# Performance work log

Measured on AMD Instinct MI355X. Metric: run time of the kernel, lower is better.

The kernel has to match this reference:

```python
import jax, jax.numpy as jnp
import numpy as np

NEG_INF = -1e15  # matches masked_fill value -1000000000000000.0
ALPHA = 0.2      # leakyReLU negative slope


def setup_inputs() -> dict:
    key = jax.random.key(0)
    k1, k2, k3, k4 = jax.random.split(key, 4)
    N, F_IN, F_OUT = 8192, 256, 64
    x = jax.random.normal(k1, (N, F_IN), dtype=jnp.float32)
    mask = jax.random.randint(k2, (N, N), 0, 2, dtype=jnp.int32)
    trans = jax.random.normal(k3, (F_IN, F_OUT), dtype=jnp.float32) * 0.1
    attn = jax.random.normal(k4, (2 * F_OUT, 1), dtype=jnp.float32) * 0.1
    return {"x": x, "mask": mask, "trans": trans, "attn": attn}


def reference(x, mask, trans, attn):
    d = trans.shape[1]
    h = x @ trans                                  # [N, d]
    e1 = h @ attn[:d, :]                           # [N, 1]
    e2 = h @ attn[d:, :]                           # [N, 1]
    scores = jax.nn.leaky_relu(e1 + e2.T, negative_slope=ALPHA)  # [N, N]
    masked = jnp.where(mask == 0, NEG_INF, scores)
    attention = jax.nn.softmax(masked, axis=1)
    return attention @ h                           # [N, d]
```

## Files before the change

### kernel.cpp

```cpp
#include <hip/hip_runtime.h>
#include <hip/hip_bf16.h>
#include <math.h>

#define N 8192
#define FIN 256
#define D 64
#define ALPHA 0.2f

typedef __attribute__((ext_vector_type(8))) short bf16x8;
typedef __attribute__((ext_vector_type(4))) float f32x4;

__global__ __launch_bounds__(256) void k_pack(
    const int* __restrict__ mask, unsigned char* __restrict__ mF)
{
    const int t = threadIdx.x;
    const int rt = blockIdx.x >> 1;
    const int half = blockIdx.x & 1;
    const int row = rt * 16 + (t >> 4);
    const int c = t & 15;
    const int m = t >> 4;
    for (int cc = half * (N / 2); cc < (half + 1) * (N / 2); cc += 128) {
        const int col = cc + c * 8;
        const int4 a = *(const int4*)(mask + (size_t)row * N + col);
        const int4 b = *(const int4*)(mask + (size_t)row * N + col + 4);
        unsigned v = (a.x != 0 ? 1u : 0u) | (a.y != 0 ? 2u : 0u)
                   | (a.z != 0 ? 4u : 0u) | (a.w != 0 ? 8u : 0u)
                   | (b.x != 0 ? 16u : 0u) | (b.y != 0 ? 32u : 0u)
                   | (b.z != 0 ? 64u : 0u) | (b.w != 0 ? 128u : 0u);
        const int cb = col >> 5;
        const int jgrp = c & 3;
        mF[((size_t)rt * 256 + cb) * 64 + jgrp * 16 + m] = (unsigned char)v;
    }
}

__global__ __launch_bounds__(256) void k_h_e(
    const float* __restrict__ x, const float* __restrict__ trans,
    const float* __restrict__ attn,
    __hip_bfloat16* __restrict__ hF, float* __restrict__ e1, float* __restrict__ e2)
{
    __shared__ float xs[8 * FIN];
    __shared__ __hip_bfloat16 hl[8 * D];
    const int t = threadIdx.x;
    const int r0 = blockIdx.x * 8;

    #pragma unroll
    for (int v = 0; v < 2; ++v) {
        int idx = t + 256 * v;
        ((float4*)xs)[idx] = ((const float4*)(x + (size_t)r0 * FIN))[idx];
    }
    __syncthreads();

    const int lane = t & 63, w = t >> 6;
    const float* xa = xs + (2 * w) * FIN;
    const float* xb = xs + (2 * w + 1) * FIN;
    float acca = 0.f, accb = 0.f;
    #pragma unroll 8
    for (int k = 0; k < FIN; ++k) {
        const float tv = trans[k * D + lane];
        acca = fmaf(xa[k], tv, acca);
        accb = fmaf(xb[k], tv, accb);
    }
    const int ra = r0 + 2 * w, rb = ra + 1;

    const float a1 = attn[lane], a2 = attn[D + lane];
    float p1a = acca * a1, p2a = acca * a2;
    float p1b = accb * a1, p2b = accb * a2;
    #pragma unroll
    for (int mm = 1; mm <= 32; mm <<= 1) {
        p1a += __shfl_xor(p1a, mm);
        p2a += __shfl_xor(p2a, mm);
        p1b += __shfl_xor(p1b, mm);
        p2b += __shfl_xor(p2b, mm);
    }
    if (lane == 0) { e1[ra] = p1a; e2[ra] = p2a; e1[rb] = p1b; e2[rb] = p2b; }

    hl[(2 * w) * D + lane]     = __float2bfloat16(acca);
    hl[(2 * w + 1) * D + lane] = __float2bfloat16(accb);
    __syncthreads();
    if (t < D) {
        const int q = t >> 4, m = t & 15;
        const int cb = r0 >> 5, jgrp = (r0 >> 3) & 3;
        union { bf16x8 v; __hip_bfloat16 h[8]; } o;
        #pragma unroll
        for (int r = 0; r < 8; ++r) o.h[r] = hl[r * D + q * 16 + m];
        *(bf16x8*)(hF + (((size_t)cb * 4 + q) * 64 + jgrp * 16 + m) * 8) = o.v;
    }
}

__global__ __launch_bounds__(256) void k_attn(
    const unsigned char* __restrict__ mF, const __hip_bfloat16* __restrict__ hF,
    const float* __restrict__ e1, const float* __restrict__ e2,
    float* __restrict__ acc_part, float* __restrict__ l_part, int cs)
{
    const int t = threadIdx.x;
    const int lane = t & 63, wave = t >> 6;
    const int i0 = (blockIdx.y * 4 + wave) * 16;
    const int rt = blockIdx.y * 4 + wave;
    const int sp = blockIdx.x;
    const int c0 = sp * cs;
    const int m = lane & 15, quad = lane >> 4;
    const int row = i0 + m;
    const float er = e1[row];

    const unsigned char* mbp = mF + ((size_t)rt * 256 + (c0 >> 5)) * 64 + lane;
    const __hip_bfloat16* hfp = hF + (((size_t)(c0 >> 5)) * 4 * 64 + lane) * 8;

    f32x4 acc0 = {0.f, 0.f, 0.f, 0.f};
    f32x4 acc1 = {0.f, 0.f, 0.f, 0.f};
    f32x4 acc2 = {0.f, 0.f, 0.f, 0.f};
    f32x4 acc3 = {0.f, 0.f, 0.f, 0.f};
    float lsum = 0.f;

    const int iters = cs >> 5;
    for (int it = 0; it < iters; ++it) {
        const int jb = c0 + it * 32 + quad * 8;
        const unsigned mc = mbp[it * 64];
        const float4 ea = *(const float4*)(e2 + jb);
        const float4 eb = *(const float4*)(e2 + jb + 4);
        const bf16x8* hq = (const bf16x8*)(hfp + (size_t)it * 2048);
        const bf16x8 b0 = hq[0];
        const bf16x8 b1 = hq[64];
        const bf16x8 b2 = hq[128];
        const bf16x8 b3 = hq[192];

        float s0 = er + ea.x; s0 = s0 > 0.f ? s0 : ALPHA * s0;
        float s1 = er + ea.y; s1 = s1 > 0.f ? s1 : ALPHA * s1;
        float s2 = er + ea.z; s2 = s2 > 0.f ? s2 : ALPHA * s2;
        float s3 = er + ea.w; s3 = s3 > 0.f ? s3 : ALPHA * s3;
        float s4 = er + eb.x; s4 = s4 > 0.f ? s4 : ALPHA * s4;
        float s5 = er + eb.y; s5 = s5 > 0.f ? s5 : ALPHA * s5;
        float s6 = er + eb.z; s6 = s6 > 0.f ? s6 : ALPHA * s6;
        float s7 = er + eb.w; s7 = s7 > 0.f ? s7 : ALPHA * s7;
        const float p0 = (mc & 1u)   ? __expf(s0) : 0.f;
        const float p1 = (mc & 2u)   ? __expf(s1) : 0.f;
        const float p2 = (mc & 4u)   ? __expf(s2) : 0.f;
        const float p3 = (mc & 8u)   ? __expf(s3) : 0.f;
        const float p4 = (mc & 16u)  ? __expf(s4) : 0.f;
        const float p5 = (mc & 32u)  ? __expf(s5) : 0.f;
        const float p6 = (mc & 64u)  ? __expf(s6) : 0.f;
        const float p7 = (mc & 128u) ? __expf(s7) : 0.f;

        union { bf16x8 v; __hip_bfloat162 h2[4]; } af;
        af.h2[0] = __float22bfloat162_rn(make_float2(p0, p1));
        af.h2[1] = __float22bfloat162_rn(make_float2(p2, p3));
        af.h2[2] = __float22bfloat162_rn(make_float2(p4, p5));
        af.h2[3] = __float22bfloat162_rn(make_float2(p6, p7));

        lsum += ((p0 + p1) + (p2 + p3)) + ((p4 + p5) + (p6 + p7));

        acc0 = __builtin_amdgcn_mfma_f32_16x16x32_bf16(af.v, b0, acc0, 0, 0, 0);
        acc1 = __builtin_amdgcn_mfma_f32_16x16x32_bf16(af.v, b1, acc1, 0, 0, 0);
        acc2 = __builtin_amdgcn_mfma_f32_16x16x32_bf16(af.v, b2, acc2, 0, 0, 0);
        acc3 = __builtin_amdgcn_mfma_f32_16x16x32_bf16(af.v, b3, acc3, 0, 0, 0);
    }

    lsum += __shfl_xor(lsum, 16);
    lsum += __shfl_xor(lsum, 32);
    if (quad == 0) l_part[(size_t)sp * N + row] = lsum;

    #pragma unroll
    for (int reg = 0; reg < 4; ++reg) {
        const size_t rbase = ((size_t)sp * N + i0 + quad * 4 + reg) * D;
        acc_part[rbase + m     ] = acc0[reg];
        acc_part[rbase + m + 16] = acc1[reg];
        acc_part[rbase + m + 32] = acc2[reg];
        acc_part[rbase + m + 48] = acc3[reg];
    }
}

__global__ __launch_bounds__(256) void k_reduce(
    const float* __restrict__ acc_part, const float* __restrict__ l_part,
    float* __restrict__ out, int nsplit)
{
    const int idx = blockIdx.x * 256 + threadIdx.x;
    const int row = idx >> 6;
    float sum = 0.f, l = 0.f;
    for (int s = 0; s < nsplit; ++s) {
        sum += acc_part[(size_t)s * N * D + idx];
        l   += l_part[(size_t)s * N + row];
    }
    out[idx] = sum / l;
}

extern "C" void kernel_launch(void* const* d_in, const int* in_sizes, int n_in,
                              void* d_out, int out_size, void* d_ws, size_t ws_size,
                              hipStream_t stream) {
    const float* x     = (const float*)d_in[0];
    const int*   mask  = (const int*)d_in[1];
    const float* trans = (const float*)d_in[2];
    const float* attn  = (const float*)d_in[3];
    float* out = (float*)d_out;

    char* ws = (char*)d_ws;
    __hip_bfloat16* hF = (__hip_bfloat16*)ws;
    char* p = ws + (size_t)D * N * sizeof(__hip_bfloat16);
    float* e1 = (float*)p;            p += (size_t)N * sizeof(float);
    float* e2 = (float*)p;            p += (size_t)N * sizeof(float);
    unsigned char* mF = (unsigned char*)p;  p += (size_t)N * (N / 8);

    const size_t used = (size_t)(p - ws);
    int nsplit = 8;
    while (nsplit > 1) {
        size_t need = used + (size_t)nsplit * N * sizeof(float)
                    + (size_t)nsplit * N * D * sizeof(float);
        if (need <= ws_size) break;
        nsplit >>= 1;
    }
    float* l_part = (float*)p;
    float* acc_part = l_part + (size_t)nsplit * N;

    k_pack<<<(N / 16) * 2, 256, 0, stream>>>(mask, mF);
    k_h_e<<<N / 8, 256, 0, stream>>>(x, trans, attn, hF, e1, e2);
    dim3 g2(nsplit, N / 64);
    k_attn<<<g2, 256, 0, stream>>>(mF, hF, e1, e2, acc_part, l_part, N / nsplit);
    k_reduce<<<(N * D) / 256, 256, 0, stream>>>(acc_part, l_part, out, nsplit);
}
```

Baseline: 427.7 us.

## Fuse mask reading into attention kernel and drop separate bit-pack pass

Removes the mask bit-packing kernel and has the attention kernel read the int32 mask directly with vector loads, so the 268MB mask goes through one pass instead of a read-then-write-then-read sequence. It also halves the column split count and unrolls the main loop by two. The attention loop now carries far more memory traffic per iteration and may become bandwidth-bound. Fewer splits reduce partial-sum traffic but also reduce grid parallelism.

```diff
diff --git a/kernel.cpp b/kernel.cpp
--- a/kernel.cpp
+++ b/kernel.cpp
@@ -9,29 +9,6 @@
 
 typedef __attribute__((ext_vector_type(8))) short bf16x8;
 typedef __attribute__((ext_vector_type(4))) float f32x4;
-
-__global__ __launch_bounds__(256) void k_pack(
-    const int* __restrict__ mask, unsigned char* __restrict__ mF)
-{
-    const int t = threadIdx.x;
-    const int rt = blockIdx.x >> 1;
-    const int half = blockIdx.x & 1;
-    const int row = rt * 16 + (t >> 4);
-    const int c = t & 15;
-    const int m = t >> 4;
-    for (int cc = half * (N / 2); cc < (half + 1) * (N / 2); cc += 128) {
-        const int col = cc + c * 8;
-        const int4 a = *(const int4*)(mask + (size_t)row * N + col);
-        const int4 b = *(const int4*)(mask + (size_t)row * N + col + 4);
-        unsigned v = (a.x != 0 ? 1u : 0u) | (a.y != 0 ? 2u : 0u)
-                   | (a.z != 0 ? 4u : 0u) | (a.w != 0 ? 8u : 0u)
-                   | (b.x != 0 ? 16u : 0u) | (b.y != 0 ? 32u : 0u)
-                   | (b.z != 0 ? 64u : 0u) | (b.w != 0 ? 128u : 0u);
-        const int cb = col >> 5;
-        const int jgrp = c & 3;
-        mF[((size_t)rt * 256 + cb) * 64 + jgrp * 16 + m] = (unsigned char)v;
-    }
-}
 
 __global__ __launch_bounds__(256) void k_h_e(
     const float* __restrict__ x, const float* __restrict__ trans,
@@ -88,21 +65,20 @@
 }
 
 __global__ __launch_bounds__(256) void k_attn(
-    const unsigned char* __restrict__ mF, const __hip_bfloat16* __restrict__ hF,
+    const int* __restrict__ mask, const __hip_bfloat16* __restrict__ hF,
     const float* __restrict__ e1, const float* __restrict__ e2,
     float* __restrict__ acc_part, float* __restrict__ l_part, int cs)
 {
     const int t = threadIdx.x;
     const int lane = t & 63, wave = t >> 6;
     const int i0 = (blockIdx.y * 4 + wave) * 16;
-    const int rt = blockIdx.y * 4 + wave;
     const int sp = blockIdx.x;
     const int c0 = sp * cs;
     const int m = lane & 15, quad = lane >> 4;
     const int row = i0 + m;
     const float er = e1[row];
+    const size_t mrow = (size_t)row * N;
 
-    const unsigned char* mbp = mF + ((size_t)rt * 256 + (c0 >> 5)) * 64 + lane;
     const __hip_bfloat16* hfp = hF + (((size_t)(c0 >> 5)) * 4 * 64 + lane) * 8;
 
     f32x4 acc0 = {0.f, 0.f, 0.f, 0.f};
@@ -112,9 +88,11 @@
     float lsum = 0.f;
 
     const int iters = cs >> 5;
+    #pragma unroll 2
     for (int it = 0; it < iters; ++it) {
         const int jb = c0 + it * 32 + quad * 8;
-        const unsigned mc = mbp[it * 64];
+        const int4   m0 = *(const int4*)(mask + mrow + jb);
+        const int4   m1 = *(const int4*)(mask + mrow + jb + 4);
         const float4 ea = *(const float4*)(e2 + jb);
         const float4 eb = *(const float4*)(e2 + jb + 4);
         const bf16x8* hq = (const bf16x8*)(hfp + (size_t)it * 2048);
@@ -131,14 +109,14 @@
         float s5 = er + eb.y; s5 = s5 > 0.f ? s5 : ALPHA * s5;
         float s6 = er + eb.z; s6 = s6 > 0.f ? s6 : ALPHA * s6;
         float s7 = er + eb.w; s7 = s7 > 0.f ? s7 : ALPHA * s7;
-        const float p0 = (mc & 1u)   ? __expf(s0) : 0.f;
-        const float p1 = (mc & 2u)   ? __expf(s1) : 0.f;
-        const float p2 = (mc & 4u)   ? __expf(s2) : 0.f;
-        const float p3 = (mc & 8u)   ? __expf(s3) : 0.f;
-        const float p4 = (mc & 16u)  ? __expf(s4) : 0.f;
-        const float p5 = (mc & 32u)  ? __expf(s5) : 0.f;
-        const float p6 = (mc & 64u)  ? __expf(s6) : 0.f;
-        const float p7 = (mc & 128u) ? __expf(s7) : 0.f;
+        const float p0 = m0.x ? __expf(s0) : 0.f;
+        const float p1 = m0.y ? __expf(s1) : 0.f;
+        const float p2 = m0.z ? __expf(s2) : 0.f;
+        const float p3 = m0.w ? __expf(s3) : 0.f;
+        const float p4 = m1.x ? __expf(s4) : 0.f;
+        const float p5 = m1.y ? __expf(s5) : 0.f;
+        const float p6 = m1.z ? __expf(s6) : 0.f;
+        const float p7 = m1.w ? __expf(s7) : 0.f;
 
         union { bf16x8 v; __hip_bfloat162 h2[4]; } af;
         af.h2[0] = __float22bfloat162_rn(make_float2(p0, p1));
@@ -196,10 +174,9 @@
     char* p = ws + (size_t)D * N * sizeof(__hip_bfloat16);
     float* e1 = (float*)p;            p += (size_t)N * sizeof(float);
     float* e2 = (float*)p;            p += (size_t)N * sizeof(float);
-    unsigned char* mF = (unsigned char*)p;  p += (size_t)N * (N / 8);
 
     const size_t used = (size_t)(p - ws);
-    int nsplit = 8;
+    int nsplit = 4;
     while (nsplit > 1) {
         size_t need = used + (size_t)nsplit * N * sizeof(float)
                     + (size_t)nsplit * N * D * sizeof(float);
@@ -209,9 +186,8 @@
     float* l_part = (float*)p;
     float* acc_part = l_part + (size_t)nsplit * N;
 
-    k_pack<<<(N / 16) * 2, 256, 0, stream>>>(mask, mF);
     k_h_e<<<N / 8, 256, 0, stream>>>(x, trans, attn, hF, e1, e2);
     dim3 g2(nsplit, N / 64);
-    k_attn<<<g2, 256, 0, stream>>>(mF, hF, e1, e2, acc_part, l_part, N / nsplit);
+    k_attn<<<g2, 256, 0, stream>>>(mask, hF, e1, e2, acc_part, l_part, N / nsplit);
     k_reduce<<<(N * D) / 256, 256, 0, stream>>>(acc_part, l_part, out, nsplit);
 }
```

New measurement: 427.9 us. Within noise of the previous version (+0.1%).
